# Kernel optimization log

Measured on AMD Instinct MI355X. Metric: run time of the kernel, lower is better.

The kernel has to match this reference:

```python
import jax, jax.numpy as jnp
import numpy as np

N_HEADS = 16

def setup_inputs() -> dict:
    key = jax.random.key(0)
    ks = jax.random.split(key, 5)
    D = 2048
    x = jax.random.normal(ks[0], (2, 2048, D), dtype=jnp.float32)
    scale = 1.0 / np.sqrt(D)
    Wq = jax.random.normal(ks[1], (D, D), dtype=jnp.float32) * scale
    Wk = jax.random.normal(ks[2], (D, D), dtype=jnp.float32) * scale
    Wv = jax.random.normal(ks[3], (D, D), dtype=jnp.float32) * scale
    Wo = jax.random.normal(ks[4], (D, D), dtype=jnp.float32) * scale
    return {"x": x, "Wq": Wq, "Wk": Wk, "Wv": Wv, "Wo": Wo}


def reference(x, Wq, Wk, Wv, Wo):
    # Causal multi-head attention. The original module computes it one query
    # position at a time (recompute loop) but the math is standard causal MHA:
    # query pos attends to key positions 0..pos.
    B, S, D = x.shape
    H = N_HEADS
    hd = D // H
    def split_heads(t):
        return t.reshape(B, S, H, hd).transpose(0, 2, 1, 3)  # (B,H,S,hd)
    q = split_heads(x @ Wq.T)
    k = split_heads(x @ Wk.T)
    v = split_heads(x @ Wv.T)
    scores = jnp.einsum('bhqd,bhkd->bhqk', q, k) / jnp.sqrt(jnp.asarray(hd, x.dtype))
    causal = jnp.tril(jnp.ones((S, S), dtype=bool))  # (S,S), True where allowed
    scores = jnp.where(causal[None, None], scores, jnp.asarray(-jnp.inf, scores.dtype))
    attn = jax.nn.softmax(scores, axis=-1)
    out = jnp.einsum('bhqk,bhkd->bhqd', attn, v)
    out = out.transpose(0, 2, 1, 3).reshape(B, S, D)
    return out @ Wo.T
```

## Files before the change

### kernel.cpp

```cpp
#include <hip/hip_runtime.h>
#include <stdint.h>

#define DD 2048
#define SS 2048
#define NB 2
#define NH 16
#define HDIM 128
#define MM (NB*SS)

typedef __attribute__((ext_vector_type(8))) short bf16x8;
typedef __attribute__((ext_vector_type(4))) float f32x4;
typedef __attribute__((ext_vector_type(4))) ushort u16x4;

__device__ __forceinline__ float fast_exp2(float x) {
  return __builtin_amdgcn_exp2f(x);
}

__device__ __forceinline__ ushort f2bf(float f) {
  union { float f; uint32_t u; } v; v.f = f;
  uint32_t u = v.u;
  return (ushort)((u + 0x7fffu + ((u >> 16) & 1u)) >> 16);
}

__device__ __forceinline__ void gld_lds16(const ushort* g, ushort* l) {
  __builtin_amdgcn_global_load_lds(
      (const __attribute__((address_space(1))) void*)g,
      (__attribute__((address_space(3))) void*)l, 16, 0, 0);
}

__global__ __launch_bounds__(256) void cvt_all(
    const float* __restrict__ x, const float* __restrict__ wq,
    const float* __restrict__ wk, const float* __restrict__ wv,
    const float* __restrict__ wo, ushort* __restrict__ dst)
{
  int i8 = blockIdx.x * 256 + threadIdx.x;
  const int X8 = MM * DD / 8;
  const int W8 = DD * DD / 8;
  const float* src; int off;
  if (i8 < X8)            { src = x;  off = i8; }
  else if (i8 < X8 +   W8){ src = wq; off = i8 - X8; }
  else if (i8 < X8 + 2*W8){ src = wk; off = i8 - (X8 +   W8); }
  else if (i8 < X8 + 3*W8){ src = wv; off = i8 - (X8 + 2*W8); }
  else                    { src = wo; off = i8 - (X8 + 3*W8); }
  const float4* p = (const float4*)src;
  float4 a = p[(long)off*2], b = p[(long)off*2 + 1];
  bf16x8 o;
  o[0]=(short)f2bf(a.x); o[1]=(short)f2bf(a.y); o[2]=(short)f2bf(a.z); o[3]=(short)f2bf(a.w);
  o[4]=(short)f2bf(b.x); o[5]=(short)f2bf(b.y); o[6]=(short)f2bf(b.z); o[7]=(short)f2bf(b.w);
  *(bf16x8*)(dst + (long)i8*8) = o;
}

template<int MODE>
__global__ __launch_bounds__(256, 2) void gemm_tri(
    const ushort* __restrict__ A, const ushort* __restrict__ Bt,
    ushort* __restrict__ Qo, ushort* __restrict__ Ko, ushort* __restrict__ Vt,
    float* __restrict__ Cf)
{
  __shared__ ushort lds[3 * 12288];
  const int t = threadIdx.x;
  const int bid = blockIdx.x;
  const int xcd = bid & 7, local = bid >> 3;
  const int NBX = (MODE == 0) ? 6 : 2;
  const int bm = local / NBX;
  const int bn = xcd * NBX + (local - bm * NBX);
  const int lane = t & 63, w = t >> 6;
  const int wr = w >> 1, wcn = w & 1;
  const int lr = lane & 15, lg = lane >> 4;

  int aoff[4], boff[2];
#pragma unroll
  for (int i = 0; i < 4; ++i) {
    int p = i*256 + t, ln = p >> 3, sr = (p & 7) ^ (ln & 7);
    aoff[i] = (2*ln + (sr >> 2)) * DD + (sr & 3) * 8;
  }
#pragma unroll
  for (int i = 0; i < 2; ++i) {
    int p = i*256 + t, ln = p >> 3, sr = (p & 7) ^ (ln & 7);
    boff[i] = (2*ln + (sr >> 2)) * DD + (sr & 3) * 8;
  }
  const ushort* Ab = A  + (long)(bm*256) * DD;
  const ushort* Bb = Bt + (long)(bn*128) * DD;

#define STG_A01(KT, BUF) do { const ushort* g_ = Ab + (KT)*32;             \
    ushort* l_ = lds + (BUF)*12288;                                        \
    gld_lds16(g_ + aoff[0], l_ + t*8);                                     \
    gld_lds16(g_ + aoff[1], l_ + (256 + t)*8); } while (0)
#define STG_A23(KT, BUF) do { const ushort* g_ = Ab + (KT)*32;             \
    ushort* l_ = lds + (BUF)*12288;                                        \
    gld_lds16(g_ + aoff[2], l_ + (512 + t)*8);                             \
    gld_lds16(g_ + aoff[3], l_ + (768 + t)*8); } while (0)
#define STG_B(KT, BUF)   do { const ushort* g_ = Bb + (KT)*32;             \
    ushort* l_ = lds + (BUF)*12288 + 8192;                                 \
    gld_lds16(g_ + boff[0], l_ + t*8);                                     \
    gld_lds16(g_ + boff[1], l_ + (256 + t)*8); } while (0)
#define LDA(dst, m) { int r_ = wr*128 + (m)*16 + lr; int ln_ = r_ >> 1;    \
    int sl_ = (lg + ((r_ & 1) << 2)) ^ (ln_ & 7);                          \
    (dst) = *(const bf16x8*)(cb + ln_*128 + sl_*16); }
#define LDB(dst, n) { int r_ = wcn*64 + (n)*16 + lr; int ln_ = r_ >> 1;    \
    int sl_ = (lg + ((r_ & 1) << 2)) ^ (ln_ & 7);                          \
    (dst) = *(const bf16x8*)(cb + 16384 + ln_*128 + sl_*16); }
#define MFMA42(AV, BV, MB, NB_) do {                                       \
    __builtin_amdgcn_s_setprio(1);                                         \
    _Pragma("unroll") for (int m = 0; m < 4; ++m)                          \
    _Pragma("unroll") for (int n = 0; n < 2; ++n)                          \
      acc[(MB)+m][(NB_)+n] = __builtin_amdgcn_mfma_f32_16x16x32_bf16(      \
          AV[m], BV[n], acc[(MB)+m][(NB_)+n], 0, 0, 0);                    \
    __builtin_amdgcn_s_setprio(0); } while (0)
#define SB  __builtin_amdgcn_sched_barrier(0)
#define BAR __builtin_amdgcn_s_barrier()
#define LGKM0 asm volatile("s_waitcnt lgkmcnt(0)" ::: "memory")

  f32x4 acc[8][4] = {};
  const int T = DD / 32;

  STG_A01(0, 0); STG_A23(0, 0); STG_B(0, 0);
  STG_A01(1, 1); STG_A23(1, 1); STG_B(1, 1);
  asm volatile("s_waitcnt vmcnt(6)" ::: "memory");
  SB; BAR; SB;

  for (int kt = 0; kt < T; ++kt) {
    const char* cb = (const char*)lds + (kt % 3) * 24576;
    const int bs = (kt + 2) % 3;
    const bool st = (kt + 2 < T);
    bf16x8 a03[4], a47[4], b01[2], b23[2];
    LDA(a03[0],0); LDA(a03[1],1); LDA(a03[2],2); LDA(a03[3],3);
    LDB(b01[0],0); LDB(b01[1],1);
    if (st) STG_A01(kt+2, bs);
    SB; BAR; LGKM0; SB;
    MFMA42(a03, b01, 0, 0);
    SB; BAR; SB;
    LDA(a47[0],4); LDA(a47[1],5); LDA(a47[2],6); LDA(a47[3],7);
    if (st) STG_A23(kt+2, bs);
    SB; BAR; LGKM0; SB;
    MFMA42(a47, b01, 4, 0);
    SB; BAR; SB;
    LDB(b23[0],2); LDB(b23[1],3);
    if (st) STG_B(kt+2, bs);
    SB; BAR; LGKM0; SB;
    MFMA42(a03, b23, 0, 2);
    SB; BAR; SB;
    if (st)              { asm volatile("s_waitcnt vmcnt(6)" ::: "memory"); }
    else if (kt + 1 < T) { asm volatile("s_waitcnt vmcnt(0)" ::: "memory"); }
    SB; BAR; SB;
    MFMA42(a47, b23, 4, 2);
    SB; BAR; SB;
  }
#undef STG_A01
#undef STG_A23
#undef STG_B
#undef LDA
#undef LDB
#undef MFMA42
#undef SB
#undef BAR
#undef LGKM0

  const int crb = bm*256 + wr*128 + lg*4;
  if (MODE == 0) {
    const int region = bn >> 4;
    const int ccb = (bn & 15)*128 + wcn*64 + lr;
    if (region < 2) {
      const float scale = (region == 0) ? (0.08838834764831845f * 1.4426950408889634f) : 1.0f;
      ushort* C = (region == 0) ? Qo : Ko;
#pragma unroll
      for (int m = 0; m < 8; ++m)
#pragma unroll
        for (int n = 0; n < 4; ++n)
#pragma unroll
          for (int j = 0; j < 4; ++j)
            C[(long)(crb + m*16 + j) * DD + (ccb + n*16)] = f2bf(acc[m][n][j] * scale);
    } else {
#pragma unroll
      for (int m = 0; m < 8; ++m) {
        int sg = crb + m*16;
        int b2 = sg >> 11, s2 = sg & 2047;
#pragma unroll
        for (int n = 0; n < 4; ++n) {
          int colv = ccb + n*16;
          int h2 = colv >> 7, d2 = colv & 127;
          u16x4 pk;
          pk[0] = f2bf(acc[m][n][0]); pk[1] = f2bf(acc[m][n][1]);
          pk[2] = f2bf(acc[m][n][2]); pk[3] = f2bf(acc[m][n][3]);
          *(u16x4*)(Vt + ((long)((b2*NH + h2)*HDIM + d2)) * SS + s2) = pk;
        }
      }
    }
  } else {
    const int ccb = bn*128 + wcn*64 + lr;
#pragma unroll
    for (int m = 0; m < 8; ++m)
#pragma unroll
      for (int n = 0; n < 4; ++n)
#pragma unroll
        for (int j = 0; j < 4; ++j)
          Cf[(long)(crb + m*16 + j) * DD + (ccb + n*16)] = acc[m][n][j];
  }
}

__global__ __launch_bounds__(512, 4) void attn_fwd(
    const ushort* __restrict__ Qb, const ushort* __restrict__ Kb,
    const ushort* __restrict__ Vtg, ushort* __restrict__ Ob)
{
  __shared__ ushort Ks[2][64*128];
  __shared__ ushort Vs[2][128*64];
  __shared__ ushort Ps[8*16*68];

  const int bid = blockIdx.x;
  const int p = bid >> 5;
  const int bh = bid & 31;
  const int b = bh >> 4, h = bh & 15;
  const int t = threadIdx.x;
  const int lane = t & 63;
  const int wq = t >> 6;
  const int lr = lane & 15, lg = lane >> 4;

  int koff0, koff1, voff0, voff1;
  { int c = t;       int kr = c >> 4, kc = c & 15; koff0 = kr*DD + ((kc ^ (kr & 7)) * 8); }
  { int c = 512 + t; int kr = c >> 4, kc = c & 15; koff1 = kr*DD + ((kc ^ (kr & 7)) * 8); }
  { int c = t;       int vd = c >> 3, vc = c & 7;  voff0 = vd*SS + ((vc ^ (vd & 7)) * 8); }
  { int c = 512 + t; int vd = c >> 3, vc = c & 7;  voff1 = vd*SS + ((vc ^ (vd & 7)) * 8); }
  const ushort* Kg = Kb + (long)(b * SS) * DD + h * HDIM;
  const ushort* Vg = Vtg + (long)(bh * HDIM) * SS;

#define STAGE(KT, BUF) do {                                   \
    const ushort* kg_ = Kg + (long)(KT) * 64 * DD;            \
    const ushort* vg_ = Vg + (KT) * 64;                       \
    gld_lds16(kg_ + koff0, &Ks[BUF][t*8]);                    \
    gld_lds16(kg_ + koff1, &Ks[BUF][4096 + t*8]);             \
    gld_lds16(vg_ + voff0, &Vs[BUF][t*8]);                    \
    gld_lds16(vg_ + voff1, &Vs[BUF][4096 + t*8]); } while (0)

  ushort* myP = Ps + wq * (16*68);
  int cur = 0;

  STAGE(0, 0);
  __syncthreads();

  for (int half = 0; half < 2; ++half) {
    const int qt = half ? (15 - p) : p;
    const int qbase = qt * 128;
    const long rowQ = (long)(b * SS + qbase + wq * 16);
    const int ntile = 2*qt + 2;
    const int qminw = qbase + wq*16;
    const int qmaxw = qminw + 15;

    bf16x8 qf[4];
#pragma unroll
    for (int c = 0; c < 4; ++c)
      qf[c] = *(const bf16x8*)(Qb + (rowQ + lr) * DD + h*HDIM + c*32 + lg*8);

    f32x4 accO[8] = {};
    float mrow[4], lrow[4];
#pragma unroll
    for (int j = 0; j < 4; ++j) { mrow[j] = -1e30f; lrow[j] = 0.f; }

    for (int kt = 0; kt < ntile; ++kt) {
      const int k0 = kt * 64;
      const bool last = (half == 1) && (kt == ntile - 1);
      if (!last) {
        const int ktn = (kt + 1 < ntile) ? (kt + 1) : 0;
        STAGE(ktn, cur ^ 1);
      }

      if (k0 <= qmaxw) {
        const ushort* Kc = Ks[cur];
        const ushort* Vc = Vs[cur];
        f32x4 sc[4] = {};
        __builtin_amdgcn_s_setprio(1);
#pragma unroll
        for (int n = 0; n < 4; ++n) {
          int r = n*16 + lr;
          int swz = (r & 7) << 4;
#pragma unroll
          for (int c = 0; c < 4; ++c) {
            bf16x8 kf = *(const bf16x8*)((const char*)Kc + ((r*256 + c*64 + lg*16) ^ swz));
            sc[n] = __builtin_amdgcn_mfma_f32_16x16x32_bf16(qf[c], kf, sc[n], 0,0,0);
          }
        }
        __builtin_amdgcn_s_setprio(0);
        if (k0 + 63 > qminw) {
#pragma unroll
          for (int n = 0; n < 4; ++n)
#pragma unroll
            for (int j = 0; j < 4; ++j) {
              int kpos = k0 + n*16 + lr;
              int qpos = qminw + lg*4 + j;
              if (kpos > qpos) sc[n][j] = -1e30f;
            }
        }
        float al[4];
#pragma unroll
        for (int j = 0; j < 4; ++j) {
          float tm = fmaxf(fmaxf(sc[0][j], sc[1][j]), fmaxf(sc[2][j], sc[3][j]));
#pragma unroll
          for (int off = 1; off < 16; off <<= 1) tm = fmaxf(tm, __shfl_xor(tm, off));
          float mn = fmaxf(mrow[j], tm);
          float a = fast_exp2(mrow[j] - mn);
          mrow[j] = mn;
          float ts = 0.f;
#pragma unroll
          for (int n = 0; n < 4; ++n) {
            float pv = fast_exp2(sc[n][j] - mn);
            sc[n][j] = pv; ts += pv;
          }
#pragma unroll
          for (int off = 1; off < 16; off <<= 1) ts += __shfl_xor(ts, off);
          lrow[j] = lrow[j] * a + ts;
          al[j] = a;
        }
#pragma unroll
        for (int dg = 0; dg < 8; ++dg) {
          f32x4 v = accO[dg];
          v[0] *= al[0]; v[1] *= al[1]; v[2] *= al[2]; v[3] *= al[3];
          accO[dg] = v;
        }
#pragma unroll
        for (int n = 0; n < 4; ++n)
#pragma unroll
          for (int j = 0; j < 4; ++j)
            myP[(lg*4 + j)*68 + n*16 + lr] = f2bf(sc[n][j]);
        bf16x8 pa0 = *(const bf16x8*)(myP + lr*68 + lg*8);
        bf16x8 pa1 = *(const bf16x8*)(myP + lr*68 + 32 + lg*8);
        __builtin_amdgcn_s_setprio(1);
#pragma unroll
        for (int dg = 0; dg < 8; ++dg) {
          int d = dg*16 + lr;
          int vswz = (d & 7) << 4;
          bf16x8 v0 = *(const bf16x8*)((const char*)Vc + ((d*128 + lg*16) ^ vswz));
          bf16x8 v1 = *(const bf16x8*)((const char*)Vc + ((d*128 + 64 + lg*16) ^ vswz));
          accO[dg] = __builtin_amdgcn_mfma_f32_16x16x32_bf16(pa0, v0, accO[dg], 0,0,0);
          accO[dg] = __builtin_amdgcn_mfma_f32_16x16x32_bf16(pa1, v1, accO[dg], 0,0,0);
        }
        __builtin_amdgcn_s_setprio(0);
      }
      __syncthreads();
      cur ^= 1;
    }

    float inv[4];
#pragma unroll
    for (int j = 0; j < 4; ++j) inv[j] = 1.0f / lrow[j];
    ushort* Og = Ob + rowQ * DD + h * HDIM;
#pragma unroll
    for (int dg = 0; dg < 8; ++dg)
#pragma unroll
      for (int j = 0; j < 4; ++j)
        Og[(long)(lg*4 + j) * DD + dg*16 + lr] = f2bf(accO[dg][j] * inv[j]);
  }
#undef STAGE
}

extern "C" void kernel_launch(void* const* d_in, const int* in_sizes, int n_in,
                              void* d_out, int out_size, void* d_ws, size_t ws_size,
                              hipStream_t stream) {
  const float* x  = (const float*)d_in[0];
  const float* Wq = (const float*)d_in[1];
  const float* Wk = (const float*)d_in[2];
  const float* Wv = (const float*)d_in[3];
  const float* Wo = (const float*)d_in[4];

  ushort* ws  = (ushort*)d_ws;
  ushort* xb  = ws;
  ushort* wqb = ws  + (long)MM*DD;
  ushort* wkb = wqb + (long)DD*DD;
  ushort* wvb = wkb + (long)DD*DD;
  ushort* wob = wvb + (long)DD*DD;
  ushort* Qb  = wob + (long)DD*DD;
  ushort* Kb  = Qb  + (long)MM*DD;
  ushort* Vtg = Kb  + (long)MM*DD;
  (void)wkb; (void)wvb;

  const int CVT_BLOCKS = (MM*DD + 4*DD*DD) / 8 / 256;
  cvt_all<<<CVT_BLOCKS, 256, 0, stream>>>(x, Wq, Wk, Wv, Wo, ws);

  gemm_tri<0><<<768, 256, 0, stream>>>(xb, wqb, Qb, Kb, Vtg, nullptr);

  attn_fwd<<<256, 512, 0, stream>>>(Qb, Kb, Vtg, xb);

  gemm_tri<1><<<256, 256, 0, stream>>>(xb, wob, nullptr, nullptr, nullptr,
                                       (float*)d_out);
}
```

Baseline: 264.4 us.

## Use 256x256-tile 8-wave GEMM kernel for fused QKV projection

Replaces the 256x128-tile, 4-wave QKV projection GEMM with a new 512-thread kernel that computes 256x256 output tiles using 128KB of double-buffered LDS and an interleaved load/MFMA schedule. The larger tile raises arithmetic intensity and halves the block count (384 instead of 768), which cuts global/L2 traffic per FLOP. In exchange the kernel uses far more LDS, which limits occupancy, relies on a fragile hand-written barrier schedule, and gives coarser load balance over the XCD-mapped grid. The output projection GEMM is simplified to keep only its fp32 store path.

```diff
diff --git a/kernel.cpp b/kernel.cpp
--- a/kernel.cpp
+++ b/kernel.cpp
@@ -50,17 +50,180 @@
   *(bf16x8*)(dst + (long)i8*8) = o;
 }
 
+__global__ __launch_bounds__(512, 2) void gemm8p(
+    const ushort* __restrict__ A, const ushort* __restrict__ Bt,
+    ushort* __restrict__ Qo, ushort* __restrict__ Ko, ushort* __restrict__ Vt)
+{
+  __shared__ char lds[131072];
+  const int t = threadIdx.x;
+  const int bid = blockIdx.x;
+  const int xcd = bid & 7, local = bid >> 3;
+  const int bm = local / 3;
+  const int bn = xcd * 3 + (local - bm*3);
+  const int lane = t & 63, w = t >> 6;
+  const int wr = w >> 2;
+  const int wcn = w & 3;
+  const int lr = lane & 15, lg = lane >> 4;
+
+  const int o0 = (t >> 3) * DD + (((t & 7) ^ ((t >> 3) & 7)) * 8);
+  const ushort* Ab = A  + (long)(bm*256) * DD;
+  const ushort* Bb = Bt + (long)(bn*256) * DD;
+
+#define STG(gbase, KT, HALF, LBYTE) do {                                   \
+    const ushort* g_ = (gbase) + (KT)*64 + (HALF)*128*DD + o0;             \
+    ushort* l_ = (ushort*)(lds + (LBYTE)) + t*8;                           \
+    gld_lds16(g_, l_);                                                     \
+    gld_lds16(g_ + 64*DD, l_ + 4096); } while (0)
+#define LDA(dst, M, ks, buf) { int r_ = (M)*16 + lr;                       \
+    (dst) = *(const bf16x8*)(lds + (buf)*65536 + wr*16384 + r_*128 +       \
+              ((((ks)*4+lg) ^ (r_ & 7)) * 16)); }
+#define LDB(dst, n, ks, buf) { int r_ = (wcn & 1)*64 + (n)*16 + lr;        \
+    (dst) = *(const bf16x8*)(lds + (buf)*65536 + 32768 + (wcn>>1)*16384 +  \
+              r_*128 + ((((ks)*4+lg) ^ (r_ & 7)) * 16)); }
+#define MFMA16(AV, BV, MB, NBASE) do {                                     \
+    __builtin_amdgcn_s_setprio(1);                                         \
+    _Pragma("unroll") for (int ks = 0; ks < 2; ++ks)                       \
+    _Pragma("unroll") for (int m = 0; m < 4; ++m)                          \
+    _Pragma("unroll") for (int n = 0; n < 2; ++n)                          \
+      acc[(MB)+m][(NBASE)+n] = __builtin_amdgcn_mfma_f32_16x16x32_bf16(    \
+          AV[m][ks], BV[n][ks], acc[(MB)+m][(NBASE)+n], 0, 0, 0);          \
+    __builtin_amdgcn_s_setprio(0); } while (0)
+#define SB  __builtin_amdgcn_sched_barrier(0)
+#define BAR __builtin_amdgcn_s_barrier()
+#define LGKM0 asm volatile("s_waitcnt lgkmcnt(0)" ::: "memory")
+#define VM4 asm volatile("s_waitcnt vmcnt(4)" ::: "memory")
+#define VM0 asm volatile("s_waitcnt vmcnt(0)" ::: "memory")
+
+  f32x4 acc[8][4] = {};
+  const int T = 32;
+
+  STG(Ab, 0, 0, 0);      STG(Ab, 0, 1, 16384);
+  STG(Bb, 0, 0, 32768);  STG(Bb, 0, 1, 49152);
+  STG(Ab, 1, 0, 65536);  STG(Ab, 1, 1, 65536+16384);
+  VM4;
+  SB; BAR; SB;
+
+  for (int i = 0; i < 16; ++i) {
+    const int a = 2*i, tb = 2*i + 1;
+    const bool st0 = (a + 2 < T);
+    const bool st1 = (tb + 2 < T);
+    bf16x8 af0[4][2], af1[4][2], bf0[2][2], bf1[2][2];
+
+#pragma unroll
+    for (int ks = 0; ks < 2; ++ks) {
+      LDA(af0[0][ks],0,ks,0); LDA(af0[1][ks],1,ks,0);
+      LDA(af0[2][ks],2,ks,0); LDA(af0[3][ks],3,ks,0);
+      LDB(bf0[0][ks],0,ks,0); LDB(bf0[1][ks],1,ks,0);
+    }
+    STG(Bb, tb, 0, 65536+32768);
+    SB; BAR; LGKM0; SB;
+    MFMA16(af0, bf0, 0, 0);
+    SB; BAR; SB;
+#pragma unroll
+    for (int ks = 0; ks < 2; ++ks) {
+      LDA(af1[0][ks],4,ks,0); LDA(af1[1][ks],5,ks,0);
+      LDA(af1[2][ks],6,ks,0); LDA(af1[3][ks],7,ks,0);
+    }
+    STG(Bb, tb, 1, 65536+49152);
+    SB; BAR; LGKM0; SB;
+    MFMA16(af1, bf0, 4, 0);
+    SB; BAR; SB;
+#pragma unroll
+    for (int ks = 0; ks < 2; ++ks) {
+      LDB(bf1[0][ks],2,ks,0); LDB(bf1[1][ks],3,ks,0);
+    }
+    if (st0) STG(Ab, a+2, 0, 0);
+    SB; BAR; LGKM0; SB;
+    MFMA16(af1, bf1, 4, 2);
+    SB; BAR; SB;
+    if (st0) { STG(Ab, a+2, 1, 16384); VM4; } else { VM0; }
+    SB; BAR; SB;
+    MFMA16(af0, bf1, 0, 2);
+    SB; BAR; SB;
+
+#pragma unroll
+    for (int ks = 0; ks < 2; ++ks) {
+      LDA(af0[0][ks],0,ks,1); LDA(af0[1][ks],1,ks,1);
+      LDA(af0[2][ks],2,ks,1); LDA(af0[3][ks],3,ks,1);
+      LDB(bf0[0][ks],0,ks,1); LDB(bf0[1][ks],1,ks,1);
+    }
+    if (st0) STG(Bb, a+2, 0, 32768);
+    SB; BAR; LGKM0; SB;
+    MFMA16(af0, bf0, 0, 0);
+    SB; BAR; SB;
+#pragma unroll
+    for (int ks = 0; ks < 2; ++ks) {
+      LDA(af1[0][ks],4,ks,1); LDA(af1[1][ks],5,ks,1);
+      LDA(af1[2][ks],6,ks,1); LDA(af1[3][ks],7,ks,1);
+    }
+    if (st0) STG(Bb, a+2, 1, 49152);
+    SB; BAR; LGKM0; SB;
+    MFMA16(af1, bf0, 4, 0);
+    SB; BAR; SB;
+#pragma unroll
+    for (int ks = 0; ks < 2; ++ks) {
+      LDB(bf1[0][ks],2,ks,1); LDB(bf1[1][ks],3,ks,1);
+    }
+    if (st1) STG(Ab, tb+2, 0, 65536);
+    SB; BAR; LGKM0; SB;
+    MFMA16(af1, bf1, 4, 2);
+    SB; BAR; SB;
+    if (st1) { STG(Ab, tb+2, 1, 65536+16384); VM4; } else { VM0; }
+    SB; BAR; SB;
+    MFMA16(af0, bf1, 0, 2);
+    SB; BAR; SB;
+  }
+#undef STG
+#undef LDA
+#undef LDB
+#undef MFMA16
+#undef SB
+#undef BAR
+#undef LGKM0
+#undef VM4
+#undef VM0
+
+  const int crb = bm*256 + wr*128 + lg*4;
+  const int region = bn >> 3;
+  const int ccb = (bn & 7)*256 + wcn*64 + lr;
+  if (region < 2) {
+    const float scale = (region == 0) ? (0.08838834764831845f * 1.4426950408889634f) : 1.0f;
+    ushort* C = (region == 0) ? Qo : Ko;
+#pragma unroll
+    for (int m = 0; m < 8; ++m)
+#pragma unroll
+      for (int n = 0; n < 4; ++n)
+#pragma unroll
+        for (int j = 0; j < 4; ++j)
+          C[(long)(crb + m*16 + j) * DD + (ccb + n*16)] = f2bf(acc[m][n][j] * scale);
+  } else {
+#pragma unroll
+    for (int m = 0; m < 8; ++m) {
+      int sg = crb + m*16;
+      int vb = sg >> 11, s2 = sg & 2047;
+#pragma unroll
+      for (int n = 0; n < 4; ++n) {
+        int colv = ccb + n*16;
+        int h2 = colv >> 7, d2 = colv & 127;
+        u16x4 pk;
+        pk[0] = f2bf(acc[m][n][0]); pk[1] = f2bf(acc[m][n][1]);
+        pk[2] = f2bf(acc[m][n][2]); pk[3] = f2bf(acc[m][n][3]);
+        *(u16x4*)(Vt + ((long)((vb*NH + h2)*HDIM + d2)) * SS + s2) = pk;
+      }
+    }
+  }
+}
+
 template<int MODE>
 __global__ __launch_bounds__(256, 2) void gemm_tri(
     const ushort* __restrict__ A, const ushort* __restrict__ Bt,
-    ushort* __restrict__ Qo, ushort* __restrict__ Ko, ushort* __restrict__ Vt,
     float* __restrict__ Cf)
 {
   __shared__ ushort lds[3 * 12288];
   const int t = threadIdx.x;
   const int bid = blockIdx.x;
   const int xcd = bid & 7, local = bid >> 3;
-  const int NBX = (MODE == 0) ? 6 : 2;
+  const int NBX = 2;
   const int bm = local / NBX;
   const int bn = xcd * NBX + (local - bm * NBX);
   const int lane = t & 63, w = t >> 6;
@@ -156,45 +319,14 @@
 #undef LGKM0
 
   const int crb = bm*256 + wr*128 + lg*4;
-  if (MODE == 0) {
-    const int region = bn >> 4;
-    const int ccb = (bn & 15)*128 + wcn*64 + lr;
-    if (region < 2) {
-      const float scale = (region == 0) ? (0.08838834764831845f * 1.4426950408889634f) : 1.0f;
-      ushort* C = (region == 0) ? Qo : Ko;
-#pragma unroll
-      for (int m = 0; m < 8; ++m)
-#pragma unroll
-        for (int n = 0; n < 4; ++n)
-#pragma unroll
-          for (int j = 0; j < 4; ++j)
-            C[(long)(crb + m*16 + j) * DD + (ccb + n*16)] = f2bf(acc[m][n][j] * scale);
-    } else {
-#pragma unroll
-      for (int m = 0; m < 8; ++m) {
-        int sg = crb + m*16;
-        int b2 = sg >> 11, s2 = sg & 2047;
-#pragma unroll
-        for (int n = 0; n < 4; ++n) {
-          int colv = ccb + n*16;
-          int h2 = colv >> 7, d2 = colv & 127;
-          u16x4 pk;
-          pk[0] = f2bf(acc[m][n][0]); pk[1] = f2bf(acc[m][n][1]);
-          pk[2] = f2bf(acc[m][n][2]); pk[3] = f2bf(acc[m][n][3]);
-          *(u16x4*)(Vt + ((long)((b2*NH + h2)*HDIM + d2)) * SS + s2) = pk;
-        }
-      }
-    }
-  } else {
-    const int ccb = bn*128 + wcn*64 + lr;
-#pragma unroll
-    for (int m = 0; m < 8; ++m)
-#pragma unroll
-      for (int n = 0; n < 4; ++n)
-#pragma unroll
-        for (int j = 0; j < 4; ++j)
-          Cf[(long)(crb + m*16 + j) * DD + (ccb + n*16)] = acc[m][n][j];
-  }
+  const int ccb = bn*128 + wcn*64 + lr;
+#pragma unroll
+  for (int m = 0; m < 8; ++m)
+#pragma unroll
+    for (int n = 0; n < 4; ++n)
+#pragma unroll
+      for (int j = 0; j < 4; ++j)
+        Cf[(long)(crb + m*16 + j) * DD + (ccb + n*16)] = acc[m][n][j];
 }
 
 __global__ __launch_bounds__(512, 4) void attn_fwd(
@@ -373,10 +505,9 @@
   const int CVT_BLOCKS = (MM*DD + 4*DD*DD) / 8 / 256;
   cvt_all<<<CVT_BLOCKS, 256, 0, stream>>>(x, Wq, Wk, Wv, Wo, ws);
 
-  gemm_tri<0><<<768, 256, 0, stream>>>(xb, wqb, Qb, Kb, Vtg, nullptr);
+  gemm8p<<<384, 512, 0, stream>>>(xb, wqb, Qb, Kb, Vtg);
 
   attn_fwd<<<256, 512, 0, stream>>>(Qb, Kb, Vtg, xb);
 
-  gemm_tri<1><<<256, 256, 0, stream>>>(xb, wob, nullptr, nullptr, nullptr,
-                                       (float*)d_out);
-}
+  gemm_tri<1><<<256, 256, 0, stream>>>(xb, wob, (float*)d_out);
+}
```

Measured after the change: 271.8 us. 2.8% more time.

## Use 128-wide KV tiles in attention with continuous double-buffer prefetch across halves

Applied to the files above, without the earlier changes.

The attention kernel now stages 128 keys and values per iteration instead of 64, which halves the number of loop iterations and block-wide barriers per query tile. The causal mask is applied only on the final diagonal tile. A single counter drives the double buffer across both query halves, so the first tile of the second half is prefetched during the first half. Shared memory grows to about 128KB per block, so the launch bound drops to 2 blocks per CU, lowering occupancy. Larger score arrays also raise register pressure, and the diagonal tile now computes some fully masked 16-row slices for warps.

```diff
diff --git a/kernel.cpp b/kernel.cpp
--- a/kernel.cpp
+++ b/kernel.cpp
@@ -197,12 +197,12 @@
   }
 }
 
-__global__ __launch_bounds__(512, 4) void attn_fwd(
+__global__ __launch_bounds__(512, 2) void attn_fwd(
     const ushort* __restrict__ Qb, const ushort* __restrict__ Kb,
     const ushort* __restrict__ Vtg, ushort* __restrict__ Ob)
 {
-  __shared__ ushort Ks[2][64*128];
-  __shared__ ushort Vs[2][128*64];
+  __shared__ ushort Ks[2][128*128];
+  __shared__ ushort Vs[2][128*128];
   __shared__ ushort Ps[8*16*68];
 
   const int bid = blockIdx.x;
@@ -214,35 +214,39 @@
   const int wq = t >> 6;
   const int lr = lane & 15, lg = lane >> 4;
 
-  int koff0, koff1, voff0, voff1;
-  { int c = t;       int kr = c >> 4, kc = c & 15; koff0 = kr*DD + ((kc ^ (kr & 7)) * 8); }
-  { int c = 512 + t; int kr = c >> 4, kc = c & 15; koff1 = kr*DD + ((kc ^ (kr & 7)) * 8); }
-  { int c = t;       int vd = c >> 3, vc = c & 7;  voff0 = vd*SS + ((vc ^ (vd & 7)) * 8); }
-  { int c = 512 + t; int vd = c >> 3, vc = c & 7;  voff1 = vd*SS + ((vc ^ (vd & 7)) * 8); }
+  int koff[4], voff[4];
+#pragma unroll
+  for (int i = 0; i < 4; ++i) {
+    int c = i*512 + t;
+    int kr = c >> 4, kc = c & 15;
+    koff[i] = kr*DD + ((kc ^ (kr & 7)) * 8);
+    voff[i] = kr*SS + ((kc ^ (kr & 7)) * 8);
+  }
   const ushort* Kg = Kb + (long)(b * SS) * DD + h * HDIM;
   const ushort* Vg = Vtg + (long)(bh * HDIM) * SS;
 
-#define STAGE(KT, BUF) do {                                   \
-    const ushort* kg_ = Kg + (long)(KT) * 64 * DD;            \
-    const ushort* vg_ = Vg + (KT) * 64;                       \
-    gld_lds16(kg_ + koff0, &Ks[BUF][t*8]);                    \
-    gld_lds16(kg_ + koff1, &Ks[BUF][4096 + t*8]);             \
-    gld_lds16(vg_ + voff0, &Vs[BUF][t*8]);                    \
-    gld_lds16(vg_ + voff1, &Vs[BUF][4096 + t*8]); } while (0)
+#define STAGE(KT, BUF) do {                                     \
+    const ushort* kg_ = Kg + (long)(KT) * 128 * DD;             \
+    const ushort* vg_ = Vg + (KT) * 128;                        \
+    _Pragma("unroll") for (int i_ = 0; i_ < 4; ++i_) {          \
+      gld_lds16(kg_ + koff[i_], &Ks[BUF][i_*4096 + t*8]);       \
+      gld_lds16(vg_ + voff[i_], &Vs[BUF][i_*4096 + t*8]);       \
+    } } while (0)
 
   ushort* myP = Ps + wq * (16*68);
-  int cur = 0;
+  const int n0 = p + 1;
+  const int TOT = 17;
 
   STAGE(0, 0);
   __syncthreads();
 
+  int u = 0;
   for (int half = 0; half < 2; ++half) {
     const int qt = half ? (15 - p) : p;
     const int qbase = qt * 128;
     const long rowQ = (long)(b * SS + qbase + wq * 16);
-    const int ntile = 2*qt + 2;
+    const int ntile = qt + 1;
     const int qminw = qbase + wq*16;
-    const int qmaxw = qminw + 15;
 
     bf16x8 qf[4];
 #pragma unroll
@@ -254,71 +258,74 @@
 #pragma unroll
     for (int j = 0; j < 4; ++j) { mrow[j] = -1e30f; lrow[j] = 0.f; }
 
-    for (int kt = 0; kt < ntile; ++kt) {
-      const int k0 = kt * 64;
-      const bool last = (half == 1) && (kt == ntile - 1);
-      if (!last) {
-        const int ktn = (kt + 1 < ntile) ? (kt + 1) : 0;
+    for (int kt = 0; kt < ntile; ++kt, ++u) {
+      const int k0 = kt * 128;
+      const int cur = u & 1;
+      if (u + 1 < TOT) {
+        const int un = u + 1;
+        const int ktn = (un < n0) ? un : un - n0;
         STAGE(ktn, cur ^ 1);
       }
 
-      if (k0 <= qmaxw) {
-        const ushort* Kc = Ks[cur];
-        const ushort* Vc = Vs[cur];
-        f32x4 sc[4] = {};
-        __builtin_amdgcn_s_setprio(1);
-#pragma unroll
-        for (int n = 0; n < 4; ++n) {
-          int r = n*16 + lr;
-          int swz = (r & 7) << 4;
-#pragma unroll
-          for (int c = 0; c < 4; ++c) {
-            bf16x8 kf = *(const bf16x8*)((const char*)Kc + ((r*256 + c*64 + lg*16) ^ swz));
-            sc[n] = __builtin_amdgcn_mfma_f32_16x16x32_bf16(qf[c], kf, sc[n], 0,0,0);
+      const ushort* Kc = Ks[cur];
+      const ushort* Vc = Vs[cur];
+      f32x4 sc[8] = {};
+      __builtin_amdgcn_s_setprio(1);
+#pragma unroll
+      for (int n = 0; n < 8; ++n) {
+        int r = n*16 + lr;
+        int swz = (r & 7) << 4;
+#pragma unroll
+        for (int c = 0; c < 4; ++c) {
+          bf16x8 kf = *(const bf16x8*)((const char*)Kc + ((r*256 + c*64 + lg*16) ^ swz));
+          sc[n] = __builtin_amdgcn_mfma_f32_16x16x32_bf16(qf[c], kf, sc[n], 0,0,0);
+        }
+      }
+      __builtin_amdgcn_s_setprio(0);
+      if (kt == ntile - 1) {
+#pragma unroll
+        for (int n = 0; n < 8; ++n)
+#pragma unroll
+          for (int j = 0; j < 4; ++j) {
+            int kpos = k0 + n*16 + lr;
+            int qpos = qminw + lg*4 + j;
+            if (kpos > qpos) sc[n][j] = -1e30f;
           }
+      }
+      float al[4];
+#pragma unroll
+      for (int j = 0; j < 4; ++j) {
+        float tm = fmaxf(fmaxf(fmaxf(sc[0][j], sc[1][j]), fmaxf(sc[2][j], sc[3][j])),
+                         fmaxf(fmaxf(sc[4][j], sc[5][j]), fmaxf(sc[6][j], sc[7][j])));
+#pragma unroll
+        for (int off = 1; off < 16; off <<= 1) tm = fmaxf(tm, __shfl_xor(tm, off));
+        float mn = fmaxf(mrow[j], tm);
+        float a = fast_exp2(mrow[j] - mn);
+        mrow[j] = mn;
+        float ts = 0.f;
+#pragma unroll
+        for (int n = 0; n < 8; ++n) {
+          float pv = fast_exp2(sc[n][j] - mn);
+          sc[n][j] = pv; ts += pv;
         }
-        __builtin_amdgcn_s_setprio(0);
-        if (k0 + 63 > qminw) {
-#pragma unroll
-          for (int n = 0; n < 4; ++n)
-#pragma unroll
-            for (int j = 0; j < 4; ++j) {
-              int kpos = k0 + n*16 + lr;
-              int qpos = qminw + lg*4 + j;
-              if (kpos > qpos) sc[n][j] = -1e30f;
-            }
-        }
-        float al[4];
-#pragma unroll
-        for (int j = 0; j < 4; ++j) {
-          float tm = fmaxf(fmaxf(sc[0][j], sc[1][j]), fmaxf(sc[2][j], sc[3][j]));
-#pragma unroll
-          for (int off = 1; off < 16; off <<= 1) tm = fmaxf(tm, __shfl_xor(tm, off));
-          float mn = fmaxf(mrow[j], tm);
-          float a = fast_exp2(mrow[j] - mn);
-          mrow[j] = mn;
-          float ts = 0.f;
-#pragma unroll
-          for (int n = 0; n < 4; ++n) {
-            float pv = fast_exp2(sc[n][j] - mn);
-            sc[n][j] = pv; ts += pv;
-          }
-#pragma unroll
-          for (int off = 1; off < 16; off <<= 1) ts += __shfl_xor(ts, off);
-          lrow[j] = lrow[j] * a + ts;
-          al[j] = a;
-        }
-#pragma unroll
-        for (int dg = 0; dg < 8; ++dg) {
-          f32x4 v = accO[dg];
-          v[0] *= al[0]; v[1] *= al[1]; v[2] *= al[2]; v[3] *= al[3];
-          accO[dg] = v;
-        }
-#pragma unroll
-        for (int n = 0; n < 4; ++n)
+#pragma unroll
+        for (int off = 1; off < 16; off <<= 1) ts += __shfl_xor(ts, off);
+        lrow[j] = lrow[j] * a + ts;
+        al[j] = a;
+      }
+#pragma unroll
+      for (int dg = 0; dg < 8; ++dg) {
+        f32x4 v = accO[dg];
+        v[0] *= al[0]; v[1] *= al[1]; v[2] *= al[2]; v[3] *= al[3];
+        accO[dg] = v;
+      }
+#pragma unroll
+      for (int hh = 0; hh < 2; ++hh) {
+#pragma unroll
+        for (int n2 = 0; n2 < 4; ++n2)
 #pragma unroll
           for (int j = 0; j < 4; ++j)
-            myP[(lg*4 + j)*68 + n*16 + lr] = f2bf(sc[n][j]);
+            myP[(lg*4 + j)*68 + n2*16 + lr] = f2bf(sc[hh*4 + n2][j]);
         bf16x8 pa0 = *(const bf16x8*)(myP + lr*68 + lg*8);
         bf16x8 pa1 = *(const bf16x8*)(myP + lr*68 + 32 + lg*8);
         __builtin_amdgcn_s_setprio(1);
@@ -326,15 +333,16 @@
         for (int dg = 0; dg < 8; ++dg) {
           int d = dg*16 + lr;
           int vswz = (d & 7) << 4;
-          bf16x8 v0 = *(const bf16x8*)((const char*)Vc + ((d*128 + lg*16) ^ vswz));
-          bf16x8 v1 = *(const bf16x8*)((const char*)Vc + ((d*128 + 64 + lg*16) ^ vswz));
+          const char* vrow = (const char*)Vc + d*256 + hh*128;
+          bf16x8 v0 = *(const bf16x8*)((const char*)Vc + ((d*256 + hh*128 + lg*16) ^ vswz));
+          bf16x8 v1 = *(const bf16x8*)((const char*)Vc + ((d*256 + hh*128 + 64 + lg*16) ^ vswz));
+          (void)vrow;
           accO[dg] = __builtin_amdgcn_mfma_f32_16x16x32_bf16(pa0, v0, accO[dg], 0,0,0);
           accO[dg] = __builtin_amdgcn_mfma_f32_16x16x32_bf16(pa1, v1, accO[dg], 0,0,0);
         }
         __builtin_amdgcn_s_setprio(0);
       }
       __syncthreads();
-      cur ^= 1;
     }
 
     float inv[4];
```

New measurement: 251.2 us (median of 2 runs). 5.0% less time.
